# Kernel optimization log

Hardware: AMD Instinct MI355X
Metric: run time of the kernel (lower is better)

Reference implementation:

```python
import jax, jax.numpy as jnp
import numpy as np
from jax import lax

B, Ht, Wt, C, NH, KV, FF = 32, 32, 32, 768, 12, 16, 4
HD = C // NH
EPS = 1e-5


def setup_inputs() -> dict:
    key = jax.random.key(0)
    ks = jax.random.split(key, 12)
    rn = lambda k, s, sc=0.02: jax.random.normal(k, s, jnp.float32) * sc
    inp = {"x": jax.random.normal(ks[0], (B, Ht * Wt, C), jnp.float32)}
    inp["ln1_g"] = jnp.ones((C,), jnp.float32)
    inp["ln1_b"] = jnp.zeros((C,), jnp.float32)
    for i, nm in enumerate(["q", "k", "v"]):
        inp[f"dw_w_{nm}"] = rn(ks[1 + i], (C, 1, 3, 3), 0.1)
        inp[f"dw_b_{nm}"] = jnp.zeros((C,), jnp.float32)
        inp[f"bn_g_{nm}"] = jnp.ones((C,), jnp.float32)
        inp[f"bn_b_{nm}"] = jnp.zeros((C,), jnp.float32)
        inp[f"bn_m_{nm}"] = jnp.zeros((C,), jnp.float32)
        inp[f"bn_v_{nm}"] = jnp.ones((C,), jnp.float32)
        inp[f"W_{nm}"] = rn(ks[4 + i], (C, C))
        inp[f"b_{nm}"] = jnp.zeros((C,), jnp.float32)
    inp["ln2_g"] = jnp.ones((C,), jnp.float32)
    inp["ln2_b"] = jnp.zeros((C,), jnp.float32)
    inp["W1"] = rn(ks[7], (FF * C, C))
    inp["b1"] = jnp.zeros((FF * C,), jnp.float32)
    inp["W2"] = rn(ks[8], (C, FF * C))
    inp["b2"] = jnp.zeros((C,), jnp.float32)
    return inp


def _ln(x, g, b):
    m = jnp.mean(x, -1, keepdims=True)
    v = jnp.var(x, -1, keepdims=True)
    return (x - m) * lax.rsqrt(v + EPS) * g + b


def _dw_branch(x4, w, bias, g, bb, m, v, stride):
    # depthwise conv (groups=C) -> ELU -> BatchNorm (eval) -> b (h w) c
    y = lax.conv_general_dilated(
        x4, w, (stride, stride), [(1, 1), (1, 1)],
        feature_group_count=C,
        dimension_numbers=("NCHW", "OIHW", "NCHW"),
    ) + bias[None, :, None, None]
    y = jax.nn.elu(y)
    y = (y - m[None, :, None, None]) * lax.rsqrt(v + EPS)[None, :, None, None] \
        * g[None, :, None, None] + bb[None, :, None, None]
    return y.reshape(B, C, -1).transpose(0, 2, 1)  # (B, n, C)


def _heads(t, Wm, bm):
    t = t @ Wm.T + bm                         # (B, n, C)
    n = t.shape[1]
    return t.reshape(B, n, NH, HD).transpose(0, 2, 1, 3)  # (B, H, n, d)


def reference(x, ln1_g, ln1_b,
              dw_w_q, dw_b_q, bn_g_q, bn_b_q, bn_m_q, bn_v_q, W_q, b_q,
              dw_w_k, dw_b_k, bn_g_k, bn_b_k, bn_m_k, bn_v_k, W_k, b_k,
              dw_w_v, dw_b_v, bn_g_v, bn_b_v, bn_m_v, bn_v_v, W_v, b_v,
              ln2_g, ln2_b, W1, b1, W2, b2):
    xn = _ln(x, ln1_g, ln1_b)
    x4 = xn.transpose(0, 2, 1).reshape(B, C, Ht, Wt)
    q = _heads(_dw_branch(x4, dw_w_q, dw_b_q, bn_g_q, bn_b_q, bn_m_q, bn_v_q, 1), W_q, b_q)
    k = _heads(_dw_branch(x4, dw_w_k, dw_b_k, bn_g_k, bn_b_k, bn_m_k, bn_v_k, 2), W_k, b_k)
    v = _heads(_dw_branch(x4, dw_w_v, dw_b_v, bn_g_v, bn_b_v, bn_m_v, bn_v_v, 2), W_v, b_v)
    scale = 1.0 / (HD ** 0.5)
    attn = jnp.einsum("bhnd,bhmd->bhnm", q, k) * scale
    attn = jax.nn.softmax(attn, axis=-1)
    o = jnp.einsum("bhnm,bhmd->bhnd", attn, v)
    o = o.transpose(0, 2, 1, 3).reshape(B, Ht * Wt, C)
    x = x + o  # DropPath is identity at inference
    h = _ln(x, ln2_g, ln2_b)
    h = jax.nn.gelu(h @ W1.T + b1, approximate=False) @ W2.T + b2
    return x + h
```

## Files before the change

### kernel.cpp

```cpp
#include <hip/hip_runtime.h>
#include <math.h>

#define NB   32
#define C_   768
#define NQ   1024
#define NKV  256
#define NH_  12
#define HD_  64
#define FFC  3072
#define EPS_ 1e-5f

typedef __attribute__((ext_vector_type(8))) _Float16 f16x8;
typedef __attribute__((ext_vector_type(4))) _Float16 f16x4;
typedef __attribute__((ext_vector_type(4))) float    f32x4;

__device__ __forceinline__ void gload_lds16(const void* g, void* l) {
  __builtin_amdgcn_global_load_lds((const __attribute__((address_space(1))) void*)g,
                                   (__attribute__((address_space(3))) void*)l, 16, 0, 0);
}

__global__ __launch_bounds__(256)
void ln_fwd_kernel(const float* __restrict__ x, const float* __restrict__ g,
                   const float* __restrict__ b, _Float16* __restrict__ out) {
  const int row = blockIdx.x;
  const float* xr = x + (size_t)row * C_;
  const int t = threadIdx.x;
  float v0 = xr[t], v1 = xr[t + 256], v2 = xr[t + 512];
  float s = v0 + v1 + v2;
  float q = v0 * v0 + v1 * v1 + v2 * v2;
#pragma unroll
  for (int m = 1; m < 64; m <<= 1) { s += __shfl_xor(s, m); q += __shfl_xor(q, m); }
  __shared__ float ls[4], lq[4];
  const int w = t >> 6, lane = t & 63;
  if (lane == 0) { ls[w] = s; lq[w] = q; }
  __syncthreads();
  s = ls[0] + ls[1] + ls[2] + ls[3];
  q = lq[0] + lq[1] + lq[2] + lq[3];
  const float mean = s * (1.f / C_);
  const float rstd = rsqrtf(q * (1.f / C_) - mean * mean + EPS_);
  _Float16* orow = out + (size_t)row * C_;
  orow[t]       = (_Float16)((v0 - mean) * rstd * g[t]       + b[t]);
  orow[t + 256] = (_Float16)((v1 - mean) * rstd * g[t + 256] + b[t + 256]);
  orow[t + 512] = (_Float16)((v2 - mean) * rstd * g[t + 512] + b[t + 512]);
}

__global__ __launch_bounds__(256)
void resln2_kernel(const float* __restrict__ x, const _Float16* __restrict__ o,
                   const float* __restrict__ g, const float* __restrict__ bb,
                   float* __restrict__ xr_out, _Float16* __restrict__ h) {
  const int row = blockIdx.x;
  const float* xp = x + (size_t)row * C_;
  const _Float16* op = o + (size_t)row * C_;
  const int t = threadIdx.x;
  float v[3]; float s = 0.f, q = 0.f;
#pragma unroll
  for (int i = 0; i < 3; i++) {
    int c = t + i * 256;
    v[i] = xp[c] + (float)op[c];
    s += v[i]; q += v[i] * v[i];
  }
#pragma unroll
  for (int m = 1; m < 64; m <<= 1) { s += __shfl_xor(s, m); q += __shfl_xor(q, m); }
  __shared__ float ls[4], lq[4];
  const int w = t >> 6, lane = t & 63;
  if (lane == 0) { ls[w] = s; lq[w] = q; }
  __syncthreads();
  s = ls[0] + ls[1] + ls[2] + ls[3];
  q = lq[0] + lq[1] + lq[2] + lq[3];
  const float mean = s * (1.f / C_);
  const float rstd = rsqrtf(q * (1.f / C_) - mean * mean + EPS_);
#pragma unroll
  for (int i = 0; i < 3; i++) {
    int c = t + i * 256;
    xr_out[(size_t)row * C_ + c] = v[i];
    h[(size_t)row * C_ + c] = (_Float16)((v[i] - mean) * rstd * g[c] + bb[c]);
  }
}

#define SZ_CC (C_ * C_)
#define SZ_CF (FFC * C_)
__global__ void cast_all_kernel(const float* __restrict__ Wq, const float* __restrict__ Wk,
                                const float* __restrict__ Wv, const float* __restrict__ W1,
                                const float* __restrict__ W2,
                                _Float16* __restrict__ oq, _Float16* __restrict__ ok,
                                _Float16* __restrict__ ov, _Float16* __restrict__ o1,
                                _Float16* __restrict__ o2) {
  const int total = 3 * SZ_CC + 2 * SZ_CF;
  int i = blockIdx.x * 256 + threadIdx.x;
  int stride = gridDim.x * 256;
  for (; i < total; i += stride) {
    if (i < SZ_CC)                     oq[i] = (_Float16)Wq[i];
    else if (i < 2 * SZ_CC)            ok[i - SZ_CC] = (_Float16)Wk[i - SZ_CC];
    else if (i < 3 * SZ_CC)            ov[i - 2 * SZ_CC] = (_Float16)Wv[i - 2 * SZ_CC];
    else if (i < 3 * SZ_CC + SZ_CF)    o1[i - 3 * SZ_CC] = (_Float16)W1[i - 3 * SZ_CC];
    else                               o2[i - 3 * SZ_CC - SZ_CF] = (_Float16)W2[i - 3 * SZ_CC - SZ_CF];
  }
}

__global__ __launch_bounds__(256)
void vtrans_kernel(const _Float16* __restrict__ vbuf, _Float16* __restrict__ vT) {
  const int b = blockIdx.z;
  const int c = blockIdx.y * 256 + threadIdx.x;
  const int kvb = blockIdx.x * 64;
#pragma unroll
  for (int kk = 0; kk < 8; kk++) {
    int kv0 = kvb + kk * 8;
    f16x8 v;
#pragma unroll
    for (int j = 0; j < 8; j++)
      v[j] = vbuf[(size_t)((b << 8) + kv0 + j) * C_ + c];
    *(f16x8*)(vT + ((size_t)(b * C_ + c) << 8) + kv0) = v;
  }
}

struct DwP { const float *w, *bias, *g, *b, *m, *v; };

__device__ __forceinline__ float elu_f(float x) {
  return x > 0.f ? x : __expf(x) - 1.f;
}

__global__ __launch_bounds__(256)
void dw_fused_kernel(const _Float16* __restrict__ xn, DwP pq, DwP pk, DwP pv,
                     _Float16* __restrict__ oq, _Float16* __restrict__ ok,
                     _Float16* __restrict__ ov) {
  const int i = blockIdx.x;
  const int b = blockIdx.z;
  const int c = blockIdx.y * 256 + threadIdx.x;
  const _Float16* xb = xn + (size_t)b * NQ * C_ + c;

  float wq[9], wk[9], wv[9];
#pragma unroll
  for (int u = 0; u < 9; u++) {
    wq[u] = pq.w[c * 9 + u]; wk[u] = pk.w[c * 9 + u]; wv[u] = pv.w[c * 9 + u];
  }
  const float skq = rsqrtf(pq.v[c] + EPS_) * pq.g[c], bnq = pq.b[c] - pq.m[c] * skq;
  const float skk = rsqrtf(pk.v[c] + EPS_) * pk.g[c], bnk = pk.b[c] - pk.m[c] * skk;
  const float skv = rsqrtf(pv.v[c] + EPS_) * pv.g[c], bnv = pv.b[c] - pv.m[c] * skv;
  const float cbq = pq.bias[c], cbk = pk.bias[c], cbv = pv.bias[c];

  float t[5][5];
  auto ldc = [&](int s, int iw) {
    const bool cv = (iw >= 0 && iw < 32);
#pragma unroll
    for (int u = 0; u < 5; u++) {
      int ih = 2 * i - 1 + u;
      t[u][s] = (cv && ih >= 0 && ih < 32) ? (float)xb[(size_t)(ih * 32 + iw) * C_] : 0.f;
    }
  };

#pragma unroll
  for (int j = 0; j < 16; j++) {
    if (j == 0) {
      ldc(0, -1); ldc(1, 0); ldc(2, 1); ldc(3, 2); ldc(4, 3);
    } else {
#pragma unroll
      for (int u = 0; u < 5; u++) { t[u][0] = t[u][2]; t[u][1] = t[u][3]; t[u][2] = t[u][4]; }
      ldc(3, 2 * j + 2); ldc(4, 2 * j + 3);
    }
    float ak = cbk, av = cbv;
#pragma unroll
    for (int u = 0; u < 3; u++)
#pragma unroll
      for (int vv = 0; vv < 3; vv++) {
        ak += t[u][vv] * wk[u * 3 + vv];
        av += t[u][vv] * wv[u * 3 + vv];
      }
    ak = elu_f(ak) * skk + bnk;
    av = elu_f(av) * skv + bnv;
    ok[((size_t)b * NKV + i * 16 + j) * C_ + c] = (_Float16)ak;
    ov[((size_t)b * NKV + i * 16 + j) * C_ + c] = (_Float16)av;
#pragma unroll
    for (int a = 0; a < 2; a++)
#pragma unroll
      for (int b2 = 0; b2 < 2; b2++) {
        float aq = cbq;
#pragma unroll
        for (int u = 0; u < 3; u++)
#pragma unroll
          for (int vv = 0; vv < 3; vv++)
            aq += t[a + u][b2 + vv] * wq[u * 3 + vv];
        aq = elu_f(aq) * skq + bnq;
        oq[((size_t)b * NQ + (2 * i + a) * 32 + (2 * j + b2)) * C_ + c] = (_Float16)aq;
      }
  }
}

__device__ __forceinline__ void stage_tile(const _Float16* __restrict__ src, int ldk,
                                           int row0, int kt, _Float16* lds, int w, int lane) {
#pragma unroll
  for (int it = 0; it < 4; it++) {
    int cid = (it * 4 + w) * 64 + lane;
    int row = cid >> 3, kg = cid & 7;
    int kgs = kg ^ (row & 7);
    const _Float16* g = src + (size_t)(row0 + row) * ldk + kt * 64 + kgs * 8;
    gload_lds16((const void*)g, (void*)((char*)lds + (it * 4 + w) * 1024));
  }
}

template <int EPI>
__global__ __launch_bounds__(256, 2)
void gemm_f16(const _Float16* __restrict__ A, const _Float16* __restrict__ Bw,
              const float* __restrict__ bias,
              _Float16* __restrict__ outh, float* __restrict__ outf,
              int M, int N, int K) {
  __shared__ __align__(16) _Float16 lds[2][2][128 * 64];
  const int tid = threadIdx.x, w = tid >> 6, lane = tid & 63;
  const int wm = w >> 1, wn = w & 1;
  const int m0 = blockIdx.x * 128, n0 = blockIdx.y * 128;

  f32x4 acc[4][4];
#pragma unroll
  for (int i = 0; i < 4; i++)
#pragma unroll
    for (int j = 0; j < 4; j++)
#pragma unroll
      for (int r = 0; r < 4; r++) acc[i][j][r] = 0.f;

  stage_tile(A, K, m0, 0, lds[0][0], w, lane);
  stage_tile(Bw, K, n0, 0, lds[0][1], w, lane);
  __syncthreads();
  const int NKT = K >> 6;
  int buf = 0;
  for (int kt = 0; kt < NKT; kt++) {
    if (kt + 1 < NKT) {
      stage_tile(A, K, m0, kt + 1, lds[buf ^ 1][0], w, lane);
      stage_tile(Bw, K, n0, kt + 1, lds[buf ^ 1][1], w, lane);
    }
    f16x8 af[4][2], bfr[4][2];
#pragma unroll
    for (int mi = 0; mi < 4; mi++)
#pragma unroll
      for (int kh = 0; kh < 2; kh++) {
        int row = wm * 64 + mi * 16 + (lane & 15);
        int kg = kh * 4 + (lane >> 4);
        af[mi][kh] = *(const f16x8*)&lds[buf][0][row * 64 + ((kg ^ (row & 7)) << 3)];
      }
#pragma unroll
    for (int ni = 0; ni < 4; ni++)
#pragma unroll
      for (int kh = 0; kh < 2; kh++) {
        int row = wn * 64 + ni * 16 + (lane & 15);
        int kg = kh * 4 + (lane >> 4);
        bfr[ni][kh] = *(const f16x8*)&lds[buf][1][row * 64 + ((kg ^ (row & 7)) << 3)];
      }
#pragma unroll
    for (int mi = 0; mi < 4; mi++)
#pragma unroll
      for (int ni = 0; ni < 4; ni++)
#pragma unroll
        for (int kh = 0; kh < 2; kh++)
          acc[mi][ni] = __builtin_amdgcn_mfma_f32_16x16x32_f16(af[mi][kh], bfr[ni][kh],
                                                               acc[mi][ni], 0, 0, 0);
    __syncthreads();
    buf ^= 1;
  }
#pragma unroll
  for (int mi = 0; mi < 4; mi++)
#pragma unroll
    for (int ni = 0; ni < 4; ni++) {
      int col = n0 + wn * 64 + ni * 16 + (lane & 15);
      float bv = bias[col];
#pragma unroll
      for (int r = 0; r < 4; r++) {
        int rowg = m0 + wm * 64 + mi * 16 + (lane >> 4) * 4 + r;
        float val = acc[mi][ni][r] + bv;
        size_t idx = (size_t)rowg * N + col;
        if (EPI == 0) {
          outh[idx] = (_Float16)val;
        } else if (EPI == 1) {
          float ge = 0.5f * val * (1.f + erff(val * 0.70710678118f));
          outh[idx] = (_Float16)ge;
        } else {
          outf[idx] += val;
        }
      }
    }
}

__global__ __launch_bounds__(512, 2)
void attn_kernel(const _Float16* __restrict__ Q, const _Float16* __restrict__ Kb,
                 const _Float16* __restrict__ vT, _Float16* __restrict__ O) {
  __shared__ __align__(16) _Float16 Klds[256 * 64];
  __shared__ __align__(16) _Float16 Vt[64 * 256];
  const int tid = threadIdx.x, w = tid >> 6, lane = tid & 63;
  const int hi = lane >> 4, lo = lane & 15;
  const int half = blockIdx.x & 1;
  const int h = (blockIdx.x >> 1) % NH_;
  const int b = blockIdx.x / (2 * NH_);

  const _Float16* qp = Q + (size_t)b * NQ * C_ + h * HD_;
  const _Float16* kp = Kb + (size_t)b * NKV * C_ + h * HD_;
  const _Float16* vp = vT + ((size_t)(b * C_ + h * HD_) << 8);

#pragma unroll
  for (int i = 0; i < 4; i++) {
    int cid = i * 512 + w * 64 + lane;
    int row = cid >> 3, kg = cid & 7;
    const _Float16* g = kp + (size_t)row * C_ + ((kg ^ (row & 7)) << 3);
    gload_lds16((const void*)g, (void*)((char*)Klds + (i * 512 + w * 64) * 16));
  }
#pragma unroll
  for (int i = 0; i < 4; i++) {
    int cid = i * 512 + w * 64 + lane;
    int row = cid >> 5, kg = cid & 31;
    const _Float16* g = vp + ((size_t)row << 8) + ((kg ^ (row & 7)) << 3);
    gload_lds16((const void*)g, (void*)((char*)Vt + (i * 512 + w * 64) * 16));
  }
  __syncthreads();

#pragma unroll
  for (int ti = 0; ti < 4; ti++) {
    const int q0 = half * 512 + w * 64 + ti * 16;
    f16x8 qf[2];
#pragma unroll
    for (int kh = 0; kh < 2; kh++)
      qf[kh] = *(const f16x8*)(qp + (size_t)(q0 + lo) * C_ + kh * 32 + hi * 8);
    f32x4 S[16];
#pragma unroll
    for (int nt = 0; nt < 16; nt++) {
      f32x4 s; s[0] = 0.f; s[1] = 0.f; s[2] = 0.f; s[3] = 0.f;
      const _Float16* krow = &Klds[(nt * 16 + lo) * 64];
#pragma unroll
      for (int kh = 0; kh < 2; kh++) {
        f16x8 kf = *(const f16x8*)&krow[((kh * 4 + hi) ^ (lo & 7)) << 3];
        s = __builtin_amdgcn_mfma_f32_16x16x32_f16(kf, qf[kh], s, 0, 0, 0);
      }
      S[nt] = s;
    }
    float mx = -1e30f;
#pragma unroll
    for (int nt = 0; nt < 16; nt++)
#pragma unroll
      for (int r = 0; r < 4; r++) { S[nt][r] *= 0.125f; mx = fmaxf(mx, S[nt][r]); }
    mx = fmaxf(mx, __shfl_xor(mx, 16));
    mx = fmaxf(mx, __shfl_xor(mx, 32));
    float sum = 0.f;
#pragma unroll
    for (int nt = 0; nt < 16; nt++)
#pragma unroll
      for (int r = 0; r < 4; r++) { float e = __expf(S[nt][r] - mx); S[nt][r] = e; sum += e; }
    sum += __shfl_xor(sum, 16);
    sum += __shfl_xor(sum, 32);
    const float inv = 1.f / sum;
    f16x8 pa8[8];
#pragma unroll
    for (int ntp = 0; ntp < 8; ntp++)
#pragma unroll
      for (int r = 0; r < 4; r++) {
        pa8[ntp][r]     = (_Float16)(S[2 * ntp][r] * inv);
        pa8[ntp][4 + r] = (_Float16)(S[2 * ntp + 1][r] * inv);
      }
    f32x4 acc[4];
#pragma unroll
    for (int dt = 0; dt < 4; dt++) { acc[dt][0] = 0.f; acc[dt][1] = 0.f; acc[dt][2] = 0.f; acc[dt][3] = 0.f; }
#pragma unroll
    for (int dt = 0; dt < 4; dt++) {
      const int d = dt * 16 + lo, sw = d & 7;
      const _Float16* vrow = &Vt[d * 256 + 4 * (hi & 1)];
#pragma unroll
      for (int ntp = 0; ntp < 8; ntp++) {
        f16x4 v0 = *(const f16x4*)&vrow[((4 * ntp + (hi >> 1)) ^ sw) << 3];
        f16x4 v1 = *(const f16x4*)&vrow[((4 * ntp + 2 + (hi >> 1)) ^ sw) << 3];
        f16x8 vt8;
#pragma unroll
        for (int r = 0; r < 4; r++) { vt8[r] = v0[r]; vt8[4 + r] = v1[r]; }
        acc[dt] = __builtin_amdgcn_mfma_f32_16x16x32_f16(pa8[ntp], vt8, acc[dt], 0, 0, 0);
      }
    }
#pragma unroll
    for (int dt = 0; dt < 4; dt++)
#pragma unroll
      for (int r = 0; r < 4; r++)
        O[(size_t)(b * NQ + q0 + 4 * hi + r) * C_ + h * HD_ + dt * 16 + lo] = (_Float16)acc[dt][r];
  }
}

extern "C" void kernel_launch(void* const* d_in, const int* in_sizes, int n_in,
                              void* d_out, int out_size, void* d_ws, size_t ws_size,
                              hipStream_t stream) {
  (void)in_sizes; (void)n_in; (void)out_size; (void)ws_size;
  const float* x    = (const float*)d_in[0];
  const float* ln1g = (const float*)d_in[1];
  const float* ln1b = (const float*)d_in[2];
  DwP pq { (const float*)d_in[3], (const float*)d_in[4], (const float*)d_in[5],
           (const float*)d_in[6], (const float*)d_in[7], (const float*)d_in[8] };
  const float* Wq = (const float*)d_in[9];  const float* bq = (const float*)d_in[10];
  DwP pk { (const float*)d_in[11], (const float*)d_in[12], (const float*)d_in[13],
           (const float*)d_in[14], (const float*)d_in[15], (const float*)d_in[16] };
  const float* Wk = (const float*)d_in[17]; const float* bk = (const float*)d_in[18];
  DwP pv { (const float*)d_in[19], (const float*)d_in[20], (const float*)d_in[21],
           (const float*)d_in[22], (const float*)d_in[23], (const float*)d_in[24] };
  const float* Wv = (const float*)d_in[25]; const float* bv = (const float*)d_in[26];
  const float* ln2g = (const float*)d_in[27];
  const float* ln2b = (const float*)d_in[28];
  const float* W1 = (const float*)d_in[29]; const float* b1 = (const float*)d_in[30];
  const float* W2 = (const float*)d_in[31]; const float* b2 = (const float*)d_in[32];

  char* ws = (char*)d_ws;
  _Float16* xn   = (_Float16*)(ws + 0);
  _Float16* o    = xn;
  _Float16* tq   = (_Float16*)(ws + 100663296);
  _Float16* tk   = (_Float16*)(ws + 150994944);
  _Float16* tv   = (_Float16*)(ws + 163577856);
  _Float16* hb   = tq;
  _Float16* vTb  = tv;
  _Float16* qb   = (_Float16*)(ws + 176160768);
  _Float16* gbuf = qb;
  _Float16* kb   = (_Float16*)(ws + 226492416);
  _Float16* vbuf = (_Float16*)(ws + 239075328);
  _Float16* wqh  = (_Float16*)(ws + 251658240);
  _Float16* wkh  = (_Float16*)(ws + 252837888);
  _Float16* wvh  = (_Float16*)(ws + 254017536);
  _Float16* w1h  = (_Float16*)(ws + 255197184);
  _Float16* w2h  = (_Float16*)(ws + 259915776);
  float* out = (float*)d_out;

  ln_fwd_kernel<<<NB * NQ, 256, 0, stream>>>(x, ln1g, ln1b, xn);
  cast_all_kernel<<<2048, 256, 0, stream>>>(Wq, Wk, Wv, W1, W2, wqh, wkh, wvh, w1h, w2h);
  dw_fused_kernel<<<dim3(16, 3, NB), 256, 0, stream>>>(xn, pq, pk, pv, tq, tk, tv);
  gemm_f16<0><<<dim3(256, 6), 256, 0, stream>>>(tq, wqh, bq, qb, nullptr, NB * NQ, C_, C_);
  gemm_f16<0><<<dim3(64, 6), 256, 0, stream>>>(tk, wkh, bk, kb, nullptr, NB * NKV, C_, C_);
  gemm_f16<0><<<dim3(64, 6), 256, 0, stream>>>(tv, wvh, bv, vbuf, nullptr, NB * NKV, C_, C_);
  vtrans_kernel<<<dim3(4, 3, NB), 256, 0, stream>>>(vbuf, vTb);
  attn_kernel<<<NB * NH_ * 2, 512, 0, stream>>>(qb, kb, vTb, o);
  resln2_kernel<<<NB * NQ, 256, 0, stream>>>(x, o, ln2g, ln2b, out, hb);
  for (int mc = 0; mc < 4; mc++) {
    gemm_f16<1><<<dim3(64, 24), 256, 0, stream>>>(hb + (size_t)mc * 8192 * C_, w1h, b1,
                                                  gbuf, nullptr, 8192, FFC, C_);
    gemm_f16<2><<<dim3(64, 6), 256, 0, stream>>>(gbuf, w2h, b2, nullptr,
                                                 out + (size_t)mc * 8192 * C_, 8192, C_, FFC);
  }
}
```

Baseline: 930.6 us.

## Vectorize depthwise conv, single-buffer GEMM for occupancy, unchunk FFN GEMMs

The depthwise conv kernel now has each thread handle two adjacent channels with half2 loads and stores, using one 384-thread block per row instead of three 256-thread blocks. The GEMM drops LDS double buffering for single buffers, asks for 3 blocks per SM and raises wave priority around the MFMA loop. This trades load/compute overlap for higher occupancy. The FFN no longer runs in four chunks: both GEMMs cover all 32768 rows in one launch each, with the workspace rearranged to hold the full GELU intermediate.

Measured after the change: 863.0 us. -7.3%, faster.

```diff
diff --git a/kernel.cpp b/kernel.cpp
--- a/kernel.cpp
+++ b/kernel.cpp
@@ -12,6 +12,7 @@
 
 typedef __attribute__((ext_vector_type(8))) _Float16 f16x8;
 typedef __attribute__((ext_vector_type(4))) _Float16 f16x4;
+typedef __attribute__((ext_vector_type(2))) _Float16 f16x2;
 typedef __attribute__((ext_vector_type(4))) float    f32x4;
 
 __device__ __forceinline__ void gload_lds16(const void* g, void* l) {
@@ -119,32 +120,42 @@
   return x > 0.f ? x : __expf(x) - 1.f;
 }
 
-__global__ __launch_bounds__(256)
+__global__ __launch_bounds__(384)
 void dw_fused_kernel(const _Float16* __restrict__ xn, DwP pq, DwP pk, DwP pv,
                      _Float16* __restrict__ oq, _Float16* __restrict__ ok,
                      _Float16* __restrict__ ov) {
   const int i = blockIdx.x;
   const int b = blockIdx.z;
-  const int c = blockIdx.y * 256 + threadIdx.x;
-  const _Float16* xb = xn + (size_t)b * NQ * C_ + c;
-
-  float wq[9], wk[9], wv[9];
+  const int c0 = 2 * threadIdx.x;
+  const _Float16* xb = xn + (size_t)b * NQ * C_ + c0;
+
+  float wqx[9], wqy[9], wkx[9], wky[9], wvx[9], wvy[9];
 #pragma unroll
   for (int u = 0; u < 9; u++) {
-    wq[u] = pq.w[c * 9 + u]; wk[u] = pk.w[c * 9 + u]; wv[u] = pv.w[c * 9 + u];
-  }
-  const float skq = rsqrtf(pq.v[c] + EPS_) * pq.g[c], bnq = pq.b[c] - pq.m[c] * skq;
-  const float skk = rsqrtf(pk.v[c] + EPS_) * pk.g[c], bnk = pk.b[c] - pk.m[c] * skk;
-  const float skv = rsqrtf(pv.v[c] + EPS_) * pv.g[c], bnv = pv.b[c] - pv.m[c] * skv;
-  const float cbq = pq.bias[c], cbk = pk.bias[c], cbv = pv.bias[c];
-
-  float t[5][5];
+    wqx[u] = pq.w[c0 * 9 + u]; wqy[u] = pq.w[(c0 + 1) * 9 + u];
+    wkx[u] = pk.w[c0 * 9 + u]; wky[u] = pk.w[(c0 + 1) * 9 + u];
+    wvx[u] = pv.w[c0 * 9 + u]; wvy[u] = pv.w[(c0 + 1) * 9 + u];
+  }
+  const float skqx = rsqrtf(pq.v[c0] + EPS_) * pq.g[c0], bnqx = pq.b[c0] - pq.m[c0] * skqx;
+  const float skqy = rsqrtf(pq.v[c0+1] + EPS_) * pq.g[c0+1], bnqy = pq.b[c0+1] - pq.m[c0+1] * skqy;
+  const float skkx = rsqrtf(pk.v[c0] + EPS_) * pk.g[c0], bnkx = pk.b[c0] - pk.m[c0] * skkx;
+  const float skky = rsqrtf(pk.v[c0+1] + EPS_) * pk.g[c0+1], bnky = pk.b[c0+1] - pk.m[c0+1] * skky;
+  const float skvx = rsqrtf(pv.v[c0] + EPS_) * pv.g[c0], bnvx = pv.b[c0] - pv.m[c0] * skvx;
+  const float skvy = rsqrtf(pv.v[c0+1] + EPS_) * pv.g[c0+1], bnvy = pv.b[c0+1] - pv.m[c0+1] * skvy;
+  const float cbqx = pq.bias[c0], cbqy = pq.bias[c0+1];
+  const float cbkx = pk.bias[c0], cbky = pk.bias[c0+1];
+  const float cbvx = pv.bias[c0], cbvy = pv.bias[c0+1];
+
+  float tx[5][5], ty[5][5];
   auto ldc = [&](int s, int iw) {
     const bool cv = (iw >= 0 && iw < 32);
 #pragma unroll
     for (int u = 0; u < 5; u++) {
       int ih = 2 * i - 1 + u;
-      t[u][s] = (cv && ih >= 0 && ih < 32) ? (float)xb[(size_t)(ih * 32 + iw) * C_] : 0.f;
+      if (cv && ih >= 0 && ih < 32) {
+        f16x2 p = *(const f16x2*)&xb[(size_t)(ih * 32 + iw) * C_];
+        tx[u][s] = (float)p[0]; ty[u][s] = (float)p[1];
+      } else { tx[u][s] = 0.f; ty[u][s] = 0.f; }
     }
   };
 
@@ -154,33 +165,43 @@
       ldc(0, -1); ldc(1, 0); ldc(2, 1); ldc(3, 2); ldc(4, 3);
     } else {
 #pragma unroll
-      for (int u = 0; u < 5; u++) { t[u][0] = t[u][2]; t[u][1] = t[u][3]; t[u][2] = t[u][4]; }
+      for (int u = 0; u < 5; u++) {
+        tx[u][0] = tx[u][2]; tx[u][1] = tx[u][3]; tx[u][2] = tx[u][4];
+        ty[u][0] = ty[u][2]; ty[u][1] = ty[u][3]; ty[u][2] = ty[u][4];
+      }
       ldc(3, 2 * j + 2); ldc(4, 2 * j + 3);
     }
-    float ak = cbk, av = cbv;
+    float akx = cbkx, aky = cbky, avx = cbvx, avy = cbvy;
 #pragma unroll
     for (int u = 0; u < 3; u++)
 #pragma unroll
       for (int vv = 0; vv < 3; vv++) {
-        ak += t[u][vv] * wk[u * 3 + vv];
-        av += t[u][vv] * wv[u * 3 + vv];
-      }
-    ak = elu_f(ak) * skk + bnk;
-    av = elu_f(av) * skv + bnv;
-    ok[((size_t)b * NKV + i * 16 + j) * C_ + c] = (_Float16)ak;
-    ov[((size_t)b * NKV + i * 16 + j) * C_ + c] = (_Float16)av;
+        akx += tx[u][vv] * wkx[u * 3 + vv]; aky += ty[u][vv] * wky[u * 3 + vv];
+        avx += tx[u][vv] * wvx[u * 3 + vv]; avy += ty[u][vv] * wvy[u * 3 + vv];
+      }
+    f16x2 kv2, vv2;
+    kv2[0] = (_Float16)(elu_f(akx) * skkx + bnkx);
+    kv2[1] = (_Float16)(elu_f(aky) * skky + bnky);
+    vv2[0] = (_Float16)(elu_f(avx) * skvx + bnvx);
+    vv2[1] = (_Float16)(elu_f(avy) * skvy + bnvy);
+    *(f16x2*)&ok[((size_t)b * NKV + i * 16 + j) * C_ + c0] = kv2;
+    *(f16x2*)&ov[((size_t)b * NKV + i * 16 + j) * C_ + c0] = vv2;
 #pragma unroll
     for (int a = 0; a < 2; a++)
 #pragma unroll
       for (int b2 = 0; b2 < 2; b2++) {
-        float aq = cbq;
+        float aqx = cbqx, aqy = cbqy;
 #pragma unroll
         for (int u = 0; u < 3; u++)
 #pragma unroll
-          for (int vv = 0; vv < 3; vv++)
-            aq += t[a + u][b2 + vv] * wq[u * 3 + vv];
-        aq = elu_f(aq) * skq + bnq;
-        oq[((size_t)b * NQ + (2 * i + a) * 32 + (2 * j + b2)) * C_ + c] = (_Float16)aq;
+          for (int vv = 0; vv < 3; vv++) {
+            aqx += tx[a + u][b2 + vv] * wqx[u * 3 + vv];
+            aqy += ty[a + u][b2 + vv] * wqy[u * 3 + vv];
+          }
+        f16x2 q2;
+        q2[0] = (_Float16)(elu_f(aqx) * skqx + bnqx);
+        q2[1] = (_Float16)(elu_f(aqy) * skqy + bnqy);
+        *(f16x2*)&oq[((size_t)b * NQ + (2 * i + a) * 32 + (2 * j + b2)) * C_ + c0] = q2;
       }
   }
 }
@@ -198,12 +219,13 @@
 }
 
 template <int EPI>
-__global__ __launch_bounds__(256, 2)
+__global__ __launch_bounds__(256, 3)
 void gemm_f16(const _Float16* __restrict__ A, const _Float16* __restrict__ Bw,
               const float* __restrict__ bias,
               _Float16* __restrict__ outh, float* __restrict__ outf,
               int M, int N, int K) {
-  __shared__ __align__(16) _Float16 lds[2][2][128 * 64];
+  __shared__ __align__(16) _Float16 As[128 * 64];
+  __shared__ __align__(16) _Float16 Bs[128 * 64];
   const int tid = threadIdx.x, w = tid >> 6, lane = tid & 63;
   const int wm = w >> 1, wn = w & 1;
   const int m0 = blockIdx.x * 128, n0 = blockIdx.y * 128;
@@ -216,16 +238,11 @@
 #pragma unroll
       for (int r = 0; r < 4; r++) acc[i][j][r] = 0.f;
 
-  stage_tile(A, K, m0, 0, lds[0][0], w, lane);
-  stage_tile(Bw, K, n0, 0, lds[0][1], w, lane);
-  __syncthreads();
   const int NKT = K >> 6;
-  int buf = 0;
   for (int kt = 0; kt < NKT; kt++) {
-    if (kt + 1 < NKT) {
-      stage_tile(A, K, m0, kt + 1, lds[buf ^ 1][0], w, lane);
-      stage_tile(Bw, K, n0, kt + 1, lds[buf ^ 1][1], w, lane);
-    }
+    stage_tile(A, K, m0, kt, As, w, lane);
+    stage_tile(Bw, K, n0, kt, Bs, w, lane);
+    __syncthreads();
     f16x8 af[4][2], bfr[4][2];
 #pragma unroll
     for (int mi = 0; mi < 4; mi++)
@@ -233,7 +250,7 @@
       for (int kh = 0; kh < 2; kh++) {
         int row = wm * 64 + mi * 16 + (lane & 15);
         int kg = kh * 4 + (lane >> 4);
-        af[mi][kh] = *(const f16x8*)&lds[buf][0][row * 64 + ((kg ^ (row & 7)) << 3)];
+        af[mi][kh] = *(const f16x8*)&As[row * 64 + ((kg ^ (row & 7)) << 3)];
       }
 #pragma unroll
     for (int ni = 0; ni < 4; ni++)
@@ -241,8 +258,9 @@
       for (int kh = 0; kh < 2; kh++) {
         int row = wn * 64 + ni * 16 + (lane & 15);
         int kg = kh * 4 + (lane >> 4);
-        bfr[ni][kh] = *(const f16x8*)&lds[buf][1][row * 64 + ((kg ^ (row & 7)) << 3)];
-      }
+        bfr[ni][kh] = *(const f16x8*)&Bs[row * 64 + ((kg ^ (row & 7)) << 3)];
+      }
+    __builtin_amdgcn_s_setprio(1);
 #pragma unroll
     for (int mi = 0; mi < 4; mi++)
 #pragma unroll
@@ -251,8 +269,8 @@
         for (int kh = 0; kh < 2; kh++)
           acc[mi][ni] = __builtin_amdgcn_mfma_f32_16x16x32_f16(af[mi][kh], bfr[ni][kh],
                                                                acc[mi][ni], 0, 0, 0);
+    __builtin_amdgcn_s_setprio(0);
     __syncthreads();
-    buf ^= 1;
   }
 #pragma unroll
   for (int mi = 0; mi < 4; mi++)
@@ -397,17 +415,17 @@
   const float* W2 = (const float*)d_in[31]; const float* b2 = (const float*)d_in[32];
 
   char* ws = (char*)d_ws;
+  _Float16* gbuf = (_Float16*)(ws + 0);
   _Float16* xn   = (_Float16*)(ws + 0);
-  _Float16* o    = xn;
-  _Float16* tq   = (_Float16*)(ws + 100663296);
-  _Float16* tk   = (_Float16*)(ws + 150994944);
-  _Float16* tv   = (_Float16*)(ws + 163577856);
+  _Float16* qb   = (_Float16*)(ws + 50331648);
+  _Float16* tk   = (_Float16*)(ws + 100663296);
+  _Float16* tv   = (_Float16*)(ws + 113246208);
+  _Float16* vTb  = tv;
+  _Float16* kb   = (_Float16*)(ws + 125829120);
+  _Float16* vbuf = (_Float16*)(ws + 138412032);
+  _Float16* o    = (_Float16*)(ws + 150994944);
+  _Float16* tq   = (_Float16*)(ws + 201326592);
   _Float16* hb   = tq;
-  _Float16* vTb  = tv;
-  _Float16* qb   = (_Float16*)(ws + 176160768);
-  _Float16* gbuf = qb;
-  _Float16* kb   = (_Float16*)(ws + 226492416);
-  _Float16* vbuf = (_Float16*)(ws + 239075328);
   _Float16* wqh  = (_Float16*)(ws + 251658240);
   _Float16* wkh  = (_Float16*)(ws + 252837888);
   _Float16* wvh  = (_Float16*)(ws + 254017536);
@@ -417,17 +435,15 @@
 
   ln_fwd_kernel<<<NB * NQ, 256, 0, stream>>>(x, ln1g, ln1b, xn);
   cast_all_kernel<<<2048, 256, 0, stream>>>(Wq, Wk, Wv, W1, W2, wqh, wkh, wvh, w1h, w2h);
-  dw_fused_kernel<<<dim3(16, 3, NB), 256, 0, stream>>>(xn, pq, pk, pv, tq, tk, tv);
+  dw_fused_kernel<<<dim3(16, 1, NB), 384, 0, stream>>>(xn, pq, pk, pv, tq, tk, tv);
   gemm_f16<0><<<dim3(256, 6), 256, 0, stream>>>(tq, wqh, bq, qb, nullptr, NB * NQ, C_, C_);
   gemm_f16<0><<<dim3(64, 6), 256, 0, stream>>>(tk, wkh, bk, kb, nullptr, NB * NKV, C_, C_);
   gemm_f16<0><<<dim3(64, 6), 256, 0, stream>>>(tv, wvh, bv, vbuf, nullptr, NB * NKV, C_, C_);
   vtrans_kernel<<<dim3(4, 3, NB), 256, 0, stream>>>(vbuf, vTb);
   attn_kernel<<<NB * NH_ * 2, 512, 0, stream>>>(qb, kb, vTb, o);
   resln2_kernel<<<NB * NQ, 256, 0, stream>>>(x, o, ln2g, ln2b, out, hb);
-  for (int mc = 0; mc < 4; mc++) {
-    gemm_f16<1><<<dim3(64, 24), 256, 0, stream>>>(hb + (size_t)mc * 8192 * C_, w1h, b1,
-                                                  gbuf, nullptr, 8192, FFC, C_);
-    gemm_f16<2><<<dim3(64, 6), 256, 0, stream>>>(gbuf, w2h, b2, nullptr,
-                                                 out + (size_t)mc * 8192 * C_, 8192, C_, FFC);
-  }
-}
+  gemm_f16<1><<<dim3(256, 24), 256, 0, stream>>>(hb, w1h, b1, gbuf, nullptr,
+                                                 NB * NQ, FFC, C_);
+  gemm_f16<2><<<dim3(256, 6), 256, 0, stream>>>(gbuf, w2h, b2, nullptr, out,
+                                                NB * NQ, C_, FFC);
+}
```
